# Kernel tuning notes

Hardware: AMD Instinct MI355X
Metric: run time of the kernel (lower is better)

## Reference

```python
import jax, jax.numpy as jnp
import numpy as np

N, E, D = 100000, 640000, 128


def _xavier(key, shape):
    return jax.random.normal(key, shape, jnp.float32) * np.float32(np.sqrt(2.0 / (shape[0] + shape[1])))


def setup_inputs() -> dict:
    key = jax.random.key(0)
    ks = jax.random.split(key, 16)
    inp = {
        "x": jax.random.normal(ks[0], (N, D), jnp.float32),
        "prompt_h": jax.random.normal(ks[1], (N, D), jnp.float32),
        "edge_attr": jax.random.normal(ks[2], (E, D), jnp.float32),
        "prompt_e": jax.random.normal(ks[3], (E, D), jnp.float32),
        "edge_index": jax.random.randint(ks[4], (2, E), 0, N, dtype=jnp.int32),
        # Linear weights stored [in, out] (torch stores [out, in]; math identical)
        "Wq": _xavier(ks[5], (D, D)), "bq": jnp.zeros((D,), jnp.float32),
        "Wk": _xavier(ks[6], (D, D)), "bk": jnp.zeros((D,), jnp.float32),
        "Wv": _xavier(ks[7], (D, D)), "bv": jnp.zeros((D,), jnp.float32),
        "We1": _xavier(ks[8], (D, D)), "be1": jnp.zeros((D,), jnp.float32),
        "We2": _xavier(ks[9], (D, D)), "be2": jnp.zeros((D,), jnp.float32),
        "Wh": _xavier(ks[10], (D, D)), "bh": jnp.zeros((D,), jnp.float32),
        "Wf1": _xavier(ks[11], (D, 2 * D)), "bf1": jnp.zeros((2 * D,), jnp.float32),
        "Wf2": _xavier(ks[12], (2 * D, D)), "bf2": jnp.zeros((D,), jnp.float32),
    }
    return inp


def reference(x, prompt_h, edge_attr, prompt_e, edge_index,
              Wq, bq, Wk, bk, Wv, bv, We1, be1, We2, be2,
              Wh, bh, Wf1, bf1, Wf2, bf2):
    relu = jax.nn.relu
    # Projections (dropout=0, eval mode)
    Q = x @ Wq + bq                      # [N, D]
    K = prompt_h @ Wk + bk               # [N, D]
    V = prompt_h @ Wv + bv               # [N, D]
    h = relu(Q * K)                      # attn_product='mul', score_act with relu
    # Edge-enhanced messages: gather source node scores per edge
    src = h[edge_index[0]]               # [E, D]
    e = relu((edge_attr + prompt_e) @ We1 + be1)
    e = relu((e + prompt_e) @ We2 + be2)  # updated edge_attr (update_e=True)
    msg = relu(src + e)                  # [E, D]
    # scatter-add aggregation into destination nodes
    aggr = jax.ops.segment_sum(msg, edge_index[1], num_segments=x.shape[0])  # [N, D]
    h_out = relu((h + V + aggr) @ Wh + bh)
    h_out = h_out + x                    # residual (in_dim == out_dim)
    h_out = relu(h_out @ Wf1 + bf1)
    h_out = h_out @ Wf2 + bf2            # [N, D]
    return h_out, e
```

## Files before the change

### kernel.cpp

```cpp
#include <hip/hip_runtime.h>

typedef __attribute__((ext_vector_type(8))) short bfrag;
typedef __attribute__((ext_vector_type(4))) float f4;

__device__ __forceinline__ unsigned short f2b(float f) {
  unsigned int u = __builtin_bit_cast(unsigned int, f);
  u = (u + 0x7fffu + ((u >> 16) & 1u)) >> 16;
  return (unsigned short)u;
}
__device__ __forceinline__ float b2f(unsigned short s) {
  unsigned int u = ((unsigned int)s) << 16;
  return __builtin_bit_cast(float, u);
}
__device__ __forceinline__ float relu(float v) { return v > 0.f ? v : 0.f; }

template <bool ADD>
__device__ __forceinline__ void stage_A(char* dst, const float* s0, const float* s1,
                                        long r0, long maxRow) {
  const int tid = threadIdx.x;
#pragma unroll
  for (int i = 0; i < 4; ++i) {
    int ch = tid + (i << 8);
    int row = ch >> 4, kg = ch & 15;
    long gr = r0 + row;
    float v[8];
    if (gr < maxRow) {
      const float4* p = (const float4*)(s0 + gr * 128 + kg * 8);
      float4 a = p[0], b = p[1];
      v[0] = a.x; v[1] = a.y; v[2] = a.z; v[3] = a.w;
      v[4] = b.x; v[5] = b.y; v[6] = b.z; v[7] = b.w;
      if (ADD) {
        const float4* q = (const float4*)(s1 + gr * 128 + kg * 8);
        float4 c = q[0], d = q[1];
        v[0] += c.x; v[1] += c.y; v[2] += c.z; v[3] += c.w;
        v[4] += d.x; v[5] += d.y; v[6] += d.z; v[7] += d.w;
      }
    } else {
#pragma unroll
      for (int j = 0; j < 8; ++j) v[j] = 0.f;
    }
    union { unsigned short h[8]; uint4 u; } pk;
#pragma unroll
    for (int j = 0; j < 8; ++j) pk.h[j] = f2b(v[j]);
    *(uint4*)(dst + (((row << 8) + (kg << 4)) ^ ((row & 7) << 4))) = pk.u;
  }
}

__device__ __forceinline__ void stage_W(char* dst, const unsigned short* src,
                                        int rowStride, int kOff) {
  const int tid = threadIdx.x;
#pragma unroll
  for (int i = 0; i < 8; ++i) {
    int ch = tid + (i << 8);
    int col = ch >> 4, kg = ch & 15;
    uint4 u = *(const uint4*)(src + (size_t)col * rowStride + kOff + kg * 8);
    *(uint4*)(dst + (((col << 8) + (kg << 4)) ^ ((col & 7) << 4))) = u;
  }
}

__device__ __forceinline__ void stage_Wh(char* dst, const unsigned short* src,
                                         int rowStride, int kOff) {
  const int tid = threadIdx.x;
#pragma unroll
  for (int i = 0; i < 4; ++i) {
    int ch = tid + (i << 8);
    int c = ch >> 3, kg = ch & 7;
    uint4 u = *(const uint4*)(src + (size_t)c * rowStride + kOff + kg * 8);
    *(uint4*)(dst + (((c << 7) + (kg << 4)) ^ ((c & 7) << 4))) = u;
  }
}

__device__ __forceinline__ void mm(const char* A, const char* W, int wm, int wn,
                                   int lane, f4 acc[2][4]) {
#pragma unroll
  for (int kk = 0; kk < 4; ++kk) {
    bfrag a[2], b[4];
#pragma unroll
    for (int rt = 0; rt < 2; ++rt) {
      int row = (wm << 5) + (rt << 4) + (lane & 15);
      a[rt] = *(const bfrag*)(A + (((row << 8) + (kk << 6) + ((lane >> 4) << 4)) ^ ((row & 7) << 4)));
    }
#pragma unroll
    for (int ct = 0; ct < 4; ++ct) {
      int col = (wn << 6) + (ct << 4) + (lane & 15);
      b[ct] = *(const bfrag*)(W + (((col << 8) + (kk << 6) + ((lane >> 4) << 4)) ^ ((col & 7) << 4)));
    }
#pragma unroll
    for (int rt = 0; rt < 2; ++rt)
#pragma unroll
      for (int ct = 0; ct < 4; ++ct)
        acc[rt][ct] = __builtin_amdgcn_mfma_f32_16x16x32_bf16(a[rt], b[ct], acc[rt][ct], 0, 0, 0);
  }
}

__device__ __forceinline__ void mm_h(const char* A, const char* W, int wm, int wn,
                                     int lane, f4 acc[2][4], int kh) {
#pragma unroll
  for (int kk2 = 0; kk2 < 2; ++kk2) {
    int kA = (kh << 1) + kk2;
    bfrag a[2], b[4];
#pragma unroll
    for (int rt = 0; rt < 2; ++rt) {
      int row = (wm << 5) + (rt << 4) + (lane & 15);
      a[rt] = *(const bfrag*)(A + (((row << 8) + (kA << 6) + ((lane >> 4) << 4)) ^ ((row & 7) << 4)));
    }
#pragma unroll
    for (int ct = 0; ct < 4; ++ct) {
      int col = (wn << 6) + (ct << 4) + (lane & 15);
      b[ct] = *(const bfrag*)(W + (((col << 7) + (kk2 << 6) + ((lane >> 4) << 4)) ^ ((col & 7) << 4)));
    }
#pragma unroll
    for (int rt = 0; rt < 2; ++rt)
#pragma unroll
      for (int ct = 0; ct < 4; ++ct)
        acc[rt][ct] = __builtin_amdgcn_mfma_f32_16x16x32_bf16(a[rt], b[ct], acc[rt][ct], 0, 0, 0);
  }
}

__global__ void k_prep(const float* __restrict__ Wq, const float* __restrict__ Wk,
                       const float* __restrict__ Wv, const float* __restrict__ We1,
                       const float* __restrict__ We2, const float* __restrict__ Wh,
                       const float* __restrict__ Wf1, const float* __restrict__ Wf2,
                       unsigned short* __restrict__ wt) {
  int b = blockIdx.x, t = threadIdx.x;
  if (b < 384) {
    int m = b >> 6;
    const float* tbl[6] = {Wq, Wk, Wv, We1, We2, Wh};
    const float* src = tbl[m];
    int local = ((b & 63) << 8) + t;
    int n = local >> 7, k = local & 127;
    wt[m * 16384 + local] = f2b(src[k * 128 + n]);
  } else if (b < 512) {
    int local = ((b - 384) << 8) + t;
    int n = local >> 7, k = local & 127;
    wt[98304 + local] = f2b(Wf1[k * 256 + n]);
  } else {
    int local = ((b - 512) << 8) + t;
    int n = local >> 8, k = local & 255;
    wt[131072 + local] = f2b(Wf2[k * 128 + n]);
  }
}

__global__ void k_deg(const int* __restrict__ ei, int* __restrict__ deg, long E) {
  long g = (long)blockIdx.x * 256 + threadIdx.x;
  if (g < E) atomicAdd(deg + ei[E + g], 1);
}

__global__ void k_scanA(const int* __restrict__ deg, int* __restrict__ ex,
                        int* __restrict__ bsum, int n) {
  __shared__ int s[256];
  int t = threadIdx.x; int g = blockIdx.x * 256 + t;
  int v = (g < n) ? deg[g] : 0;
  int val = v;
  s[t] = val; __syncthreads();
#pragma unroll
  for (int o = 1; o < 256; o <<= 1) {
    int u = (t >= o) ? s[t - o] : 0;
    __syncthreads();
    val += u; s[t] = val;
    __syncthreads();
  }
  if (g < n) ex[g] = val - v;
  if (t == 255) bsum[blockIdx.x] = val;
}

__global__ void k_scanB(int* __restrict__ bsum, int nb) {
  __shared__ int s[1024];
  int t = threadIdx.x;
  int v = (t < nb) ? bsum[t] : 0;
  int val = v;
  s[t] = val; __syncthreads();
#pragma unroll
  for (int o = 1; o < 1024; o <<= 1) {
    int u = (t >= o) ? s[t - o] : 0;
    __syncthreads();
    val += u; s[t] = val;
    __syncthreads();
  }
  if (t < nb) bsum[t] = val - v;
}

__global__ void k_scanC(const int* __restrict__ ex, const int* __restrict__ bsum,
                        int* __restrict__ off, int* __restrict__ cursor, int n) {
  int g = blockIdx.x * 256 + threadIdx.x;
  if (g < n) {
    int o = ex[g] + bsum[blockIdx.x];
    off[g] = o; cursor[g] = o;
  }
}

__global__ void k_fill(const int* __restrict__ ei, int* __restrict__ cursor,
                       int* __restrict__ eidx, long E) {
  long g = (long)blockIdx.x * 256 + threadIdx.x;
  if (g < E) {
    int pos = atomicAdd(cursor + ei[E + g], 1);
    eidx[pos] = (int)g;
  }
}

__global__ __launch_bounds__(256, 2) void k_nodes1(
    const float* __restrict__ x, const float* __restrict__ ph,
    const float* __restrict__ bq, const float* __restrict__ bk,
    const float* __restrict__ bv, const unsigned short* __restrict__ wt,
    unsigned short* __restrict__ hbf, float* __restrict__ hpv, long N) {
  extern __shared__ char sm[];
  char* Ax = sm;
  char* Aph = sm + 16384;
  char* Wl = sm + 32768;
  long n0 = (long)blockIdx.x * 64;
  stage_A<false>(Ax, x, nullptr, n0, N);
  stage_A<false>(Aph, ph, nullptr, n0, N);
  stage_W(Wl, wt + 0, 128, 0);
  __syncthreads();
  const int tid = threadIdx.x, lane = tid & 63, w = tid >> 6, wm = w >> 1, wn = w & 1;
  f4 accQ[2][4] = {};
  mm(Ax, Wl, wm, wn, lane, accQ);
  __syncthreads();
  stage_W(Wl, wt + 16384, 128, 0);
  __syncthreads();
  f4 accK[2][4] = {};
  mm(Aph, Wl, wm, wn, lane, accK);
  __syncthreads();
  stage_W(Wl, wt + 32768, 128, 0);
  __syncthreads();
  f4 accV[2][4] = {};
  mm(Aph, Wl, wm, wn, lane, accV);
#pragma unroll
  for (int ct = 0; ct < 4; ++ct) {
    int col = (wn << 6) + (ct << 4) + (lane & 15);
    float vbq = bq[col], vbk = bk[col], vbv = bv[col];
#pragma unroll
    for (int rt = 0; rt < 2; ++rt)
#pragma unroll
      for (int j = 0; j < 4; ++j) {
        int rl = (wm << 5) + (rt << 4) + ((lane >> 4) << 2) + j;
        long row = n0 + rl;
        if (row < N) {
          float q = accQ[rt][ct][j] + vbq;
          float k = accK[rt][ct][j] + vbk;
          float v = accV[rt][ct][j] + vbv;
          float h = relu(q * k);
          hbf[row * 128 + col] = f2b(h);
          hpv[row * 128 + col] = h + v;
        }
      }
  }
}

__global__ __launch_bounds__(256, 3) void k_edges(
    const float* __restrict__ ea, const float* __restrict__ pe,
    const float* __restrict__ be1, const float* __restrict__ be2,
    const unsigned short* __restrict__ wt, const int* __restrict__ ei,
    const unsigned short* __restrict__ hbf, unsigned short* __restrict__ msg,
    float* __restrict__ eout, long E) {
  extern __shared__ char sm[];
  char* A = sm;
  unsigned short* peL = (unsigned short*)(sm + 16384);
  char* Wl = sm + 32768;
  char* stg = sm + 16384;
  int* srcI = (int*)(sm + 49152);
  const int tid = threadIdx.x;
  long e0 = (long)blockIdx.x * 64;
  if (tid < 64) srcI[tid] = (e0 + tid < E) ? ei[e0 + tid] : 0;
#pragma unroll
  for (int i = 0; i < 4; ++i) {
    int ch = tid + (i << 8);
    int row = ch >> 4, kg = ch & 15;
    long gr = e0 + row;
    union { unsigned short h[8]; uint4 u; } s, q;
    if (gr < E) {
      const float4* pa = (const float4*)(ea + gr * 128 + kg * 8);
      const float4* pp = (const float4*)(pe + gr * 128 + kg * 8);
      float4 a0 = pa[0], a1 = pa[1];
      float4 p0 = pp[0], p1 = pp[1];
      s.h[0] = f2b(a0.x + p0.x); s.h[1] = f2b(a0.y + p0.y);
      s.h[2] = f2b(a0.z + p0.z); s.h[3] = f2b(a0.w + p0.w);
      s.h[4] = f2b(a1.x + p1.x); s.h[5] = f2b(a1.y + p1.y);
      s.h[6] = f2b(a1.z + p1.z); s.h[7] = f2b(a1.w + p1.w);
      q.h[0] = f2b(p0.x); q.h[1] = f2b(p0.y); q.h[2] = f2b(p0.z); q.h[3] = f2b(p0.w);
      q.h[4] = f2b(p1.x); q.h[5] = f2b(p1.y); q.h[6] = f2b(p1.z); q.h[7] = f2b(p1.w);
    } else {
      s.u = uint4{0, 0, 0, 0}; q.u = uint4{0, 0, 0, 0};
    }
    *(uint4*)((char*)peL + (row << 8) + (kg << 4)) = q.u;
    *(uint4*)(A + (((row << 8) + (kg << 4)) ^ ((row & 7) << 4))) = s.u;
  }
  stage_Wh(Wl, wt + 49152, 128, 0);
  __syncthreads();
  const int lane = tid & 63, w = tid >> 6, wm = w >> 1, wn = w & 1;
  f4 acc[2][4] = {};
  mm_h(A, Wl, wm, wn, lane, acc, 0);
  __syncthreads();
  stage_Wh(Wl, wt + 49152, 128, 64);
  __syncthreads();
  mm_h(A, Wl, wm, wn, lane, acc, 1);
  __syncthreads();
  const int c0 = (tid & 31) << 2;
  const float4 vb1 = *(const float4*)(be1 + c0);
#pragma unroll
  for (int h = 0; h < 2; ++h) {
    if (wm == h) {
#pragma unroll
      for (int ct = 0; ct < 4; ++ct) {
        int col = (wn << 6) + (ct << 4) + (lane & 15);
#pragma unroll
        for (int rt = 0; rt < 2; ++rt)
#pragma unroll
          for (int j = 0; j < 4; ++j) {
            int lr = (rt << 4) + ((lane >> 4) << 2) + j;
            *(float*)(Wl + (((lr << 9) + (col << 2)) ^ ((lr & 7) << 4))) = acc[rt][ct][j];
          }
      }
    }
    __syncthreads();
#pragma unroll
    for (int it = 0; it < 4; ++it) {
      int lr = (tid >> 5) + (it << 3);
      int r = (h << 5) + lr;
      f4 a = *(const f4*)(Wl + (((lr << 9) + (c0 << 2)) ^ ((lr & 7) << 4)));
      uint2 pu = *(const uint2*)(peL + (r << 7) + c0);
      float p0 = b2f((unsigned short)pu.x), p1 = b2f((unsigned short)(pu.x >> 16));
      float p2 = b2f((unsigned short)pu.y), p3 = b2f((unsigned short)(pu.y >> 16));
      unsigned short t0 = f2b(relu(a[0] + vb1.x) + p0);
      unsigned short t1 = f2b(relu(a[1] + vb1.y) + p1);
      unsigned short t2 = f2b(relu(a[2] + vb1.z) + p2);
      unsigned short t3 = f2b(relu(a[3] + vb1.w) + p3);
      uint2 op;
      op.x = (unsigned int)t0 | ((unsigned int)t1 << 16);
      op.y = (unsigned int)t2 | ((unsigned int)t3 << 16);
      *(uint2*)(A + (((r << 8) + (c0 << 1)) ^ ((r & 7) << 4))) = op;
    }
    __syncthreads();
  }
  stage_Wh(Wl, wt + 65536, 128, 0);
  __syncthreads();
  f4 acc2[2][4] = {};
  mm_h(A, Wl, wm, wn, lane, acc2, 0);
  __syncthreads();
  stage_Wh(Wl, wt + 65536, 128, 64);
  __syncthreads();
  mm_h(A, Wl, wm, wn, lane, acc2, 1);
  __syncthreads();
#pragma unroll
  for (int ct = 0; ct < 4; ++ct) {
    int col = (wn << 6) + (ct << 4) + (lane & 15);
#pragma unroll
    for (int rt = 0; rt < 2; ++rt)
#pragma unroll
      for (int j = 0; j < 4; ++j) {
        int rl = (wm << 5) + (rt << 4) + ((lane >> 4) << 2) + j;
        *(float*)(stg + (((rl << 9) + (col << 2)) ^ ((rl & 7) << 4))) = acc2[rt][ct][j];
      }
  }
  __syncthreads();
  const float4 vb2 = *(const float4*)(be2 + c0);
#pragma unroll
  for (int it = 0; it < 8; ++it) {
    int r = (tid >> 5) + (it << 3);
    long edge = e0 + r;
    if (edge < E) {
      f4 a = *(const f4*)(stg + (((r << 9) + (c0 << 2)) ^ ((r & 7) << 4)));
      float ev0 = relu(a[0] + vb2.x), ev1 = relu(a[1] + vb2.y);
      float ev2 = relu(a[2] + vb2.z), ev3 = relu(a[3] + vb2.w);
      float4 ov; ov.x = ev0; ov.y = ev1; ov.z = ev2; ov.w = ev3;
      *(float4*)(eout + edge * 128 + c0) = ov;
      uint2 hu = *(const uint2*)(hbf + (long)srcI[r] * 128 + c0);
      float h0 = b2f((unsigned short)hu.x), h1 = b2f((unsigned short)(hu.x >> 16));
      float h2 = b2f((unsigned short)hu.y), h3 = b2f((unsigned short)(hu.y >> 16));
      unsigned short m0 = f2b(relu(ev0 + h0)), m1 = f2b(relu(ev1 + h1));
      unsigned short m2 = f2b(relu(ev2 + h2)), m3 = f2b(relu(ev3 + h3));
      uint2 mo;
      mo.x = (unsigned int)m0 | ((unsigned int)m1 << 16);
      mo.y = (unsigned int)m2 | ((unsigned int)m3 << 16);
      *(uint2*)(msg + edge * 128 + c0) = mo;
    }
  }
}

__global__ __launch_bounds__(256, 2) void k_edges_at(
    const float* __restrict__ ea, const float* __restrict__ pe,
    const float* __restrict__ be1, const float* __restrict__ be2,
    const unsigned short* __restrict__ wt, const int* __restrict__ ei,
    const unsigned short* __restrict__ hbf, float* __restrict__ aggr,
    float* __restrict__ eout, long E) {
  extern __shared__ char sm[];
  char* A = sm;
  unsigned short* peL = (unsigned short*)(sm + 16384);
  char* Wl = sm + 32768;
  int* srcI = (int*)(sm + 65536);
  int* dstI = srcI + 64;
  const int tid = threadIdx.x;
  long e0 = (long)blockIdx.x * 64;
  if (tid < 64) {
    long ge = e0 + tid;
    srcI[tid] = (ge < E) ? ei[ge] : 0;
    dstI[tid] = (ge < E) ? ei[E + ge] : 0;
  }
#pragma unroll
  for (int i = 0; i < 4; ++i) {
    int ch = tid + (i << 8);
    int row = ch >> 4, kg = ch & 15;
    long gr = e0 + row;
    union { unsigned short h[8]; uint4 u; } s, q;
    if (gr < E) {
      const float4* pa = (const float4*)(ea + gr * 128 + kg * 8);
      const float4* pp = (const float4*)(pe + gr * 128 + kg * 8);
      float4 a0 = pa[0], a1 = pa[1];
      float4 p0 = pp[0], p1 = pp[1];
      s.h[0] = f2b(a0.x + p0.x); s.h[1] = f2b(a0.y + p0.y);
      s.h[2] = f2b(a0.z + p0.z); s.h[3] = f2b(a0.w + p0.w);
      s.h[4] = f2b(a1.x + p1.x); s.h[5] = f2b(a1.y + p1.y);
      s.h[6] = f2b(a1.z + p1.z); s.h[7] = f2b(a1.w + p1.w);
      q.h[0] = f2b(p0.x); q.h[1] = f2b(p0.y); q.h[2] = f2b(p0.z); q.h[3] = f2b(p0.w);
      q.h[4] = f2b(p1.x); q.h[5] = f2b(p1.y); q.h[6] = f2b(p1.z); q.h[7] = f2b(p1.w);
    } else {
      s.u = uint4{0, 0, 0, 0}; q.u = uint4{0, 0, 0, 0};
    }
    *(uint4*)((char*)peL + (row << 8) + (kg << 4)) = q.u;
    *(uint4*)(A + (((row << 8) + (kg << 4)) ^ ((row & 7) << 4))) = s.u;
  }
  stage_W(Wl, wt + 49152, 128, 0);
  __syncthreads();
  const int lane = tid & 63, w = tid >> 6, wm = w >> 1, wn = w & 1;
  f4 acc[2][4] = {};
  mm(A, Wl, wm, wn, lane, acc);
  __syncthreads();
#pragma unroll
  for (int ct = 0; ct < 4; ++ct) {
    int col = (wn << 6) + (ct << 4) + (lane & 15);
    float b1 = be1[col];
#pragma unroll
    for (int rt = 0; rt < 2; ++rt)
#pragma unroll
      for (int j = 0; j < 4; ++j) {
        int rl = (wm << 5) + (rt << 4) + ((lane >> 4) << 2) + j;
        float tv = relu(acc[rt][ct][j] + b1) + b2f(peL[rl * 128 + col]);
        *(unsigned short*)(A + (((rl << 8) + (col << 1)) ^ ((rl & 7) << 4))) = f2b(tv);
      }
  }
  stage_W(Wl, wt + 65536, 128, 0);
  __syncthreads();
  f4 acc2[2][4] = {};
  mm(A, Wl, wm, wn, lane, acc2);
#pragma unroll
  for (int ct = 0; ct < 4; ++ct) {
    int col = (wn << 6) + (ct << 4) + (lane & 15);
    float b2 = be2[col];
#pragma unroll
    for (int rt = 0; rt < 2; ++rt)
#pragma unroll
      for (int j = 0; j < 4; ++j) {
        int rl = (wm << 5) + (rt << 4) + ((lane >> 4) << 2) + j;
        long edge = e0 + rl;
        if (edge < E) {
          float ev = relu(acc2[rt][ct][j] + b2);
          eout[edge * 128 + col] = ev;
          float hs = b2f(hbf[(long)srcI[rl] * 128 + col]);
          float m = relu(ev + hs);
          atomicAdd(aggr + (long)dstI[rl] * 128 + col, m);
        }
      }
  }
}

__global__ __launch_bounds__(256) void k_aggr(
    const int* __restrict__ off, const int* __restrict__ deg,
    const int* __restrict__ eidx, const unsigned short* __restrict__ msg,
    float* __restrict__ aggr, long N) {
  long node = (long)blockIdx.x * 4 + (threadIdx.x >> 6);
  if (node >= N) return;
  const int lane = threadIdx.x & 63;
  int st = off[node], d = deg[node];
  float a0 = 0.f, a1 = 0.f;
  for (int i = 0; i < d; ++i) {
    int eid = eidx[st + i];
    unsigned int u = *(const unsigned int*)(msg + (long)eid * 128 + lane * 2);
    a0 += b2f((unsigned short)u);
    a1 += b2f((unsigned short)(u >> 16));
  }
  *(float2*)(aggr + node * 128 + lane * 2) = float2{a0, a1};
}

__global__ __launch_bounds__(256, 2) void k_nodes2(
    const float* __restrict__ hpv, const float* __restrict__ aggr,
    const float* __restrict__ x, const float* __restrict__ bh,
    const float* __restrict__ bf1, const float* __restrict__ bf2,
    const unsigned short* __restrict__ wt, float* __restrict__ out, long N) {
  extern __shared__ char sm[];
  char* A = sm;
  char* T = sm + 16384;
  char* Wl = sm + 32768;
  long n0 = (long)blockIdx.x * 64;
  const int tid = threadIdx.x;
  stage_A<true>(A, hpv, aggr, n0, N);
  stage_W(Wl, wt + 81920, 128, 0);
  __syncthreads();
  const int lane = tid & 63, w = tid >> 6, wm = w >> 1, wn = w & 1;
  f4 acc1[2][4] = {};
  mm(A, Wl, wm, wn, lane, acc1);
  __syncthreads();
#pragma unroll
  for (int ct = 0; ct < 4; ++ct) {
    int col = (wn << 6) + (ct << 4) + (lane & 15);
    float bb = bh[col];
#pragma unroll
    for (int rt = 0; rt < 2; ++rt)
#pragma unroll
      for (int j = 0; j < 4; ++j) {
        int rl = (wm << 5) + (rt << 4) + ((lane >> 4) << 2) + j;
        long row = n0 + rl;
        float xv = (row < N) ? x[row * 128 + col] : 0.f;
        float tv = relu(acc1[rt][ct][j] + bb) + xv;
        *(unsigned short*)(T + (((rl << 8) + (col << 1)) ^ ((rl & 7) << 4))) = f2b(tv);
      }
  }
  stage_W(Wl, wt + 98304, 128, 0);
  __syncthreads();
  f4 accA[2][4] = {};
  mm(T, Wl, wm, wn, lane, accA);
  __syncthreads();
#pragma unroll
  for (int ct = 0; ct < 4; ++ct) {
    int col = (wn << 6) + (ct << 4) + (lane & 15);
    float bb = bf1[col];
#pragma unroll
    for (int rt = 0; rt < 2; ++rt)
#pragma unroll
      for (int j = 0; j < 4; ++j) {
        int rl = (wm << 5) + (rt << 4) + ((lane >> 4) << 2) + j;
        float uv = relu(accA[rt][ct][j] + bb);
        *(unsigned short*)(A + (((rl << 8) + (col << 1)) ^ ((rl & 7) << 4))) = f2b(uv);
      }
  }
  stage_W(Wl, wt + 131072, 256, 0);
  __syncthreads();
  f4 acc3[2][4] = {};
  mm(A, Wl, wm, wn, lane, acc3);
  __syncthreads();
  stage_W(Wl, wt + 114688, 128, 0);
  __syncthreads();
  f4 accB[2][4] = {};
  mm(T, Wl, wm, wn, lane, accB);
  __syncthreads();
#pragma unroll
  for (int ct = 0; ct < 4; ++ct) {
    int col = (wn << 6) + (ct << 4) + (lane & 15);
    float bb = bf1[128 + col];
#pragma unroll
    for (int rt = 0; rt < 2; ++rt)
#pragma unroll
      for (int j = 0; j < 4; ++j) {
        int rl = (wm << 5) + (rt << 4) + ((lane >> 4) << 2) + j;
        float uv = relu(accB[rt][ct][j] + bb);
        *(unsigned short*)(A + (((rl << 8) + (col << 1)) ^ ((rl & 7) << 4))) = f2b(uv);
      }
  }
  stage_W(Wl, wt + 131072, 256, 128);
  __syncthreads();
  mm(A, Wl, wm, wn, lane, acc3);
#pragma unroll
  for (int ct = 0; ct < 4; ++ct) {
    int col = (wn << 6) + (ct << 4) + (lane & 15);
    float bb = bf2[col];
#pragma unroll
    for (int rt = 0; rt < 2; ++rt)
#pragma unroll
      for (int j = 0; j < 4; ++j) {
        int rl = (wm << 5) + (rt << 4) + ((lane >> 4) << 2) + j;
        long row = n0 + rl;
        if (row < N) out[row * 128 + col] = acc3[rt][ct][j] + bb;
      }
  }
}

extern "C" void kernel_launch(void* const* d_in, const int* in_sizes, int n_in,
                              void* d_out, int out_size, void* d_ws, size_t ws_size,
                              hipStream_t stream) {
  const float* x   = (const float*)d_in[0];
  const float* ph  = (const float*)d_in[1];
  const float* ea  = (const float*)d_in[2];
  const float* pe  = (const float*)d_in[3];
  const int*   ei  = (const int*)d_in[4];
  const float* Wq  = (const float*)d_in[5];  const float* bq  = (const float*)d_in[6];
  const float* Wk  = (const float*)d_in[7];  const float* bk  = (const float*)d_in[8];
  const float* Wv  = (const float*)d_in[9];  const float* bv  = (const float*)d_in[10];
  const float* We1 = (const float*)d_in[11]; const float* be1 = (const float*)d_in[12];
  const float* We2 = (const float*)d_in[13]; const float* be2 = (const float*)d_in[14];
  const float* Wh  = (const float*)d_in[15]; const float* bh  = (const float*)d_in[16];
  const float* Wf1 = (const float*)d_in[17]; const float* bf1 = (const float*)d_in[18];
  const float* Wf2 = (const float*)d_in[19]; const float* bf2 = (const float*)d_in[20];
  const long N = in_sizes[0] / 128;
  const long E = in_sizes[2] / 128;

  char* ws = (char*)d_ws;
  size_t pos = 0;
  auto alloc = [&](size_t bytes) { size_t p = pos; pos += (bytes + 255) & ~255ULL; return p; };
  size_t o_wt   = alloc(327680);
  size_t o_hbf  = alloc((size_t)N * 256);
  size_t o_hpv  = alloc((size_t)N * 512);
  size_t o_aggr = alloc((size_t)N * 512);
  size_t base_needed = pos;
  size_t o_deg  = alloc((size_t)N * 4);
  size_t o_ex   = alloc((size_t)N * 4);
  size_t o_cur  = alloc((size_t)N * 4);
  size_t o_off  = alloc((size_t)N * 4);
  size_t o_bsum = alloc(4096);
  size_t o_eidx = alloc((size_t)E * 4);
  size_t o_msg  = alloc((size_t)E * 256);
  size_t csr_needed = pos;
  (void)base_needed;

  unsigned short* wt  = (unsigned short*)(ws + o_wt);
  unsigned short* hbf = (unsigned short*)(ws + o_hbf);
  float* hpv  = (float*)(ws + o_hpv);
  float* aggr = (float*)(ws + o_aggr);
  float* outH = (float*)d_out;
  float* outE = outH + N * 128;

  k_prep<<<640, 256, 0, stream>>>(Wq, Wk, Wv, We1, We2, Wh, Wf1, Wf2, wt);
  int nb = (int)((N + 63) / 64);
  int eb = (int)((E + 63) / 64);
  k_nodes1<<<nb, 256, 65536, stream>>>(x, ph, bq, bk, bv, wt, hbf, hpv, N);

  if (ws_size >= csr_needed) {
    int* deg = (int*)(ws + o_deg);
    int* ex  = (int*)(ws + o_ex);
    int* cur = (int*)(ws + o_cur);
    int* off = (int*)(ws + o_off);
    int* bsum = (int*)(ws + o_bsum);
    int* eidx = (int*)(ws + o_eidx);
    unsigned short* msg = (unsigned short*)(ws + o_msg);
    int nb1 = (int)((N + 255) / 256);
    hipMemsetAsync(deg, 0, (size_t)N * 4, stream);
    k_deg<<<(int)((E + 255) / 256), 256, 0, stream>>>(ei, deg, E);
    k_scanA<<<nb1, 256, 0, stream>>>(deg, ex, bsum, (int)N);
    k_scanB<<<1, 1024, 0, stream>>>(bsum, nb1);
    k_scanC<<<nb1, 256, 0, stream>>>(ex, bsum, off, cur, (int)N);
    k_fill<<<(int)((E + 255) / 256), 256, 0, stream>>>(ei, cur, eidx, E);
    k_edges<<<eb, 256, 49408, stream>>>(ea, pe, be1, be2, wt, ei, hbf, msg, outE, E);
    k_aggr<<<(int)((N + 3) / 4), 256, 0, stream>>>(off, deg, eidx, msg, aggr, N);
  } else {
    hipMemsetAsync(aggr, 0, (size_t)N * 512, stream);
    k_edges_at<<<eb, 256, 66048, stream>>>(ea, pe, be1, be2, wt, ei, hbf, aggr, outE, E);
  }
  k_nodes2<<<nb, 256, 65536, stream>>>(hpv, aggr, x, bh, bf1, bf2, wt, outH, N);
}
```

Before: 624.4 us.

## Store h+V in bf16, coalesce node stores, prefetch gathers, unroll aggregation

k_nodes1 now stages its h and h+V outputs through shared memory and writes them as coalesced 8-byte chunks. h+V is stored in bf16 instead of fp32, which halves that intermediate's traffic but adds a rounding step before the Wh matmul. k_edges issues the source-node gathers of h at kernel start so their latency overlaps the edge matmuls. k_aggr unrolls its neighbour loop by four to keep more loads in flight. The atomic fallback path is removed and the CSR path always runs.

```diff
diff --git a/kernel.cpp b/kernel.cpp
--- a/kernel.cpp
+++ b/kernel.cpp
@@ -14,9 +14,7 @@
 }
 __device__ __forceinline__ float relu(float v) { return v > 0.f ? v : 0.f; }
 
-template <bool ADD>
-__device__ __forceinline__ void stage_A(char* dst, const float* s0, const float* s1,
-                                        long r0, long maxRow) {
+__device__ __forceinline__ void stage_A(char* dst, const float* s0, long r0, long maxRow) {
   const int tid = threadIdx.x;
 #pragma unroll
   for (int i = 0; i < 4; ++i) {
@@ -29,12 +27,6 @@
       float4 a = p[0], b = p[1];
       v[0] = a.x; v[1] = a.y; v[2] = a.z; v[3] = a.w;
       v[4] = b.x; v[5] = b.y; v[6] = b.z; v[7] = b.w;
-      if (ADD) {
-        const float4* q = (const float4*)(s1 + gr * 128 + kg * 8);
-        float4 c = q[0], d = q[1];
-        v[0] += c.x; v[1] += c.y; v[2] += c.z; v[3] += c.w;
-        v[4] += d.x; v[5] += d.y; v[6] += d.z; v[7] += d.w;
-      }
     } else {
 #pragma unroll
       for (int j = 0; j < 8; ++j) v[j] = 0.f;
@@ -42,6 +34,34 @@
     union { unsigned short h[8]; uint4 u; } pk;
 #pragma unroll
     for (int j = 0; j < 8; ++j) pk.h[j] = f2b(v[j]);
+    *(uint4*)(dst + (((row << 8) + (kg << 4)) ^ ((row & 7) << 4))) = pk.u;
+  }
+}
+
+__device__ __forceinline__ void stage_A_mix(char* dst, const unsigned short* hb,
+                                            const float* ag, long r0, long maxRow) {
+  const int tid = threadIdx.x;
+#pragma unroll
+  for (int i = 0; i < 4; ++i) {
+    int ch = tid + (i << 8);
+    int row = ch >> 4, kg = ch & 15;
+    long gr = r0 + row;
+    union { unsigned short h[8]; uint4 u; } pk;
+    if (gr < maxRow) {
+      uint4 hv = *(const uint4*)(hb + gr * 128 + kg * 8);
+      const float4* q = (const float4*)(ag + gr * 128 + kg * 8);
+      float4 c = q[0], d = q[1];
+      pk.h[0] = f2b(b2f((unsigned short)hv.x) + c.x);
+      pk.h[1] = f2b(b2f((unsigned short)(hv.x >> 16)) + c.y);
+      pk.h[2] = f2b(b2f((unsigned short)hv.y) + c.z);
+      pk.h[3] = f2b(b2f((unsigned short)(hv.y >> 16)) + c.w);
+      pk.h[4] = f2b(b2f((unsigned short)hv.z) + d.x);
+      pk.h[5] = f2b(b2f((unsigned short)(hv.z >> 16)) + d.y);
+      pk.h[6] = f2b(b2f((unsigned short)hv.w) + d.z);
+      pk.h[7] = f2b(b2f((unsigned short)(hv.w >> 16)) + d.w);
+    } else {
+      pk.u = uint4{0, 0, 0, 0};
+    }
     *(uint4*)(dst + (((row << 8) + (kg << 4)) ^ ((row & 7) << 4))) = pk.u;
   }
 }
@@ -114,6 +134,34 @@
 #pragma unroll
       for (int ct = 0; ct < 4; ++ct)
         acc[rt][ct] = __builtin_amdgcn_mfma_f32_16x16x32_bf16(a[rt], b[ct], acc[rt][ct], 0, 0, 0);
+  }
+}
+
+__device__ __forceinline__ void dump_half(char* Wl, const f4 acc[2][4], int lane, int wn) {
+#pragma unroll
+  for (int ct = 0; ct < 4; ++ct) {
+    int col = (wn << 6) + (ct << 4) + (lane & 15);
+#pragma unroll
+    for (int rt = 0; rt < 2; ++rt)
+#pragma unroll
+      for (int j = 0; j < 4; ++j) {
+        int lr = (rt << 4) + ((lane >> 4) << 2) + j;
+        *(float*)(Wl + (((lr << 9) + (col << 2)) ^ ((lr & 7) << 4))) = acc[rt][ct][j];
+      }
+  }
+}
+
+__device__ __forceinline__ void dump_full(char* stg, const f4 acc[2][4], int lane, int wm, int wn) {
+#pragma unroll
+  for (int ct = 0; ct < 4; ++ct) {
+    int col = (wn << 6) + (ct << 4) + (lane & 15);
+#pragma unroll
+    for (int rt = 0; rt < 2; ++rt)
+#pragma unroll
+      for (int j = 0; j < 4; ++j) {
+        int rl = (wm << 5) + (rt << 4) + ((lane >> 4) << 2) + j;
+        *(float*)(stg + (((rl << 9) + (col << 2)) ^ ((rl & 7) << 4))) = acc[rt][ct][j];
+      }
   }
 }
 
@@ -202,17 +250,18 @@
     const float* __restrict__ x, const float* __restrict__ ph,
     const float* __restrict__ bq, const float* __restrict__ bk,
     const float* __restrict__ bv, const unsigned short* __restrict__ wt,
-    unsigned short* __restrict__ hbf, float* __restrict__ hpv, long N) {
+    unsigned short* __restrict__ hbf, unsigned short* __restrict__ hpvb, long N) {
   extern __shared__ char sm[];
   char* Ax = sm;
   char* Aph = sm + 16384;
   char* Wl = sm + 32768;
   long n0 = (long)blockIdx.x * 64;
-  stage_A<false>(Ax, x, nullptr, n0, N);
-  stage_A<false>(Aph, ph, nullptr, n0, N);
+  const int tid = threadIdx.x, lane = tid & 63, w = tid >> 6, wm = w >> 1, wn = w & 1;
+  const int team = tid >> 5, c0 = (tid & 31) << 2;
+  stage_A(Ax, x, n0, N);
+  stage_A(Aph, ph, n0, N);
   stage_W(Wl, wt + 0, 128, 0);
   __syncthreads();
-  const int tid = threadIdx.x, lane = tid & 63, w = tid >> 6, wm = w >> 1, wn = w & 1;
   f4 accQ[2][4] = {};
   mm(Ax, Wl, wm, wn, lane, accQ);
   __syncthreads();
@@ -225,6 +274,7 @@
   __syncthreads();
   f4 accV[2][4] = {};
   mm(Aph, Wl, wm, wn, lane, accV);
+  __syncthreads();
 #pragma unroll
   for (int ct = 0; ct < 4; ++ct) {
     int col = (wn << 6) + (ct << 4) + (lane & 15);
@@ -234,16 +284,25 @@
 #pragma unroll
       for (int j = 0; j < 4; ++j) {
         int rl = (wm << 5) + (rt << 4) + ((lane >> 4) << 2) + j;
-        long row = n0 + rl;
-        if (row < N) {
-          float q = accQ[rt][ct][j] + vbq;
-          float k = accK[rt][ct][j] + vbk;
-          float v = accV[rt][ct][j] + vbv;
-          float h = relu(q * k);
-          hbf[row * 128 + col] = f2b(h);
-          hpv[row * 128 + col] = h + v;
-        }
+        float q = accQ[rt][ct][j] + vbq;
+        float k = accK[rt][ct][j] + vbk;
+        float v = accV[rt][ct][j] + vbv;
+        float h = relu(q * k);
+        *(unsigned short*)(Ax + (((rl << 8) + (col << 1)) ^ ((rl & 7) << 4))) = f2b(h);
+        *(unsigned short*)(Aph + (((rl << 8) + (col << 1)) ^ ((rl & 7) << 4))) = f2b(h + v);
       }
+  }
+  __syncthreads();
+#pragma unroll
+  for (int it = 0; it < 8; ++it) {
+    int r = team + (it << 3);
+    long row = n0 + r;
+    if (row < N) {
+      uint2 hb = *(const uint2*)(Ax + (((r << 8) + (c0 << 1)) ^ ((r & 7) << 4)));
+      uint2 hv = *(const uint2*)(Aph + (((r << 8) + (c0 << 1)) ^ ((r & 7) << 4)));
+      *(uint2*)(hbf + row * 128 + c0) = hb;
+      *(uint2*)(hpvb + row * 128 + c0) = hv;
+    }
   }
 }
 
@@ -258,10 +317,18 @@
   unsigned short* peL = (unsigned short*)(sm + 16384);
   char* Wl = sm + 32768;
   char* stg = sm + 16384;
-  int* srcI = (int*)(sm + 49152);
   const int tid = threadIdx.x;
+  const int team = tid >> 5, c0 = (tid & 31) << 2;
   long e0 = (long)blockIdx.x * 64;
-  if (tid < 64) srcI[tid] = (e0 + tid < E) ? ei[e0 + tid] : 0;
+
+  uint2 hu[8];
+#pragma unroll
+  for (int it = 0; it < 8; ++it) {
+    int r = team + (it << 3);
+    long ge = e0 + r;
+    int s = (ge < E) ? ei[ge] : 0;
+    hu[it] = *(const uint2*)(hbf + (long)s * 128 + c0);
+  }
 #pragma unroll
   for (int i = 0; i < 4; ++i) {
     int ch = tid + (i << 8);
@@ -295,27 +362,14 @@
   __syncthreads();
   mm_h(A, Wl, wm, wn, lane, acc, 1);
   __syncthreads();
-  const int c0 = (tid & 31) << 2;
   const float4 vb1 = *(const float4*)(be1 + c0);
 #pragma unroll
   for (int h = 0; h < 2; ++h) {
-    if (wm == h) {
-#pragma unroll
-      for (int ct = 0; ct < 4; ++ct) {
-        int col = (wn << 6) + (ct << 4) + (lane & 15);
-#pragma unroll
-        for (int rt = 0; rt < 2; ++rt)
-#pragma unroll
-          for (int j = 0; j < 4; ++j) {
-            int lr = (rt << 4) + ((lane >> 4) << 2) + j;
-            *(float*)(Wl + (((lr << 9) + (col << 2)) ^ ((lr & 7) << 4))) = acc[rt][ct][j];
-          }
-      }
-    }
+    if (wm == h) dump_half(Wl, acc, lane, wn);
     __syncthreads();
 #pragma unroll
     for (int it = 0; it < 4; ++it) {
-      int lr = (tid >> 5) + (it << 3);
+      int lr = team + (it << 3);
       int r = (h << 5) + lr;
       f4 a = *(const f4*)(Wl + (((lr << 9) + (c0 << 2)) ^ ((lr & 7) << 4)));
       uint2 pu = *(const uint2*)(peL + (r << 7) + c0);
@@ -341,22 +395,12 @@
   __syncthreads();
   mm_h(A, Wl, wm, wn, lane, acc2, 1);
   __syncthreads();
-#pragma unroll
-  for (int ct = 0; ct < 4; ++ct) {
-    int col = (wn << 6) + (ct << 4) + (lane & 15);
-#pragma unroll
-    for (int rt = 0; rt < 2; ++rt)
-#pragma unroll
-      for (int j = 0; j < 4; ++j) {
-        int rl = (wm << 5) + (rt << 4) + ((lane >> 4) << 2) + j;
-        *(float*)(stg + (((rl << 9) + (col << 2)) ^ ((rl & 7) << 4))) = acc2[rt][ct][j];
-      }
-  }
+  dump_full(stg, acc2, lane, wm, wn);
   __syncthreads();
   const float4 vb2 = *(const float4*)(be2 + c0);
 #pragma unroll
   for (int it = 0; it < 8; ++it) {
-    int r = (tid >> 5) + (it << 3);
+    int r = team + (it << 3);
     long edge = e0 + r;
     if (edge < E) {
       f4 a = *(const f4*)(stg + (((r << 9) + (c0 << 2)) ^ ((r & 7) << 4)));
@@ -364,9 +408,8 @@
       float ev2 = relu(a[2] + vb2.z), ev3 = relu(a[3] + vb2.w);
       float4 ov; ov.x = ev0; ov.y = ev1; ov.z = ev2; ov.w = ev3;
       *(float4*)(eout + edge * 128 + c0) = ov;
-      uint2 hu = *(const uint2*)(hbf + (long)srcI[r] * 128 + c0);
-      float h0 = b2f((unsigned short)hu.x), h1 = b2f((unsigned short)(hu.x >> 16));
-      float h2 = b2f((unsigned short)hu.y), h3 = b2f((unsigned short)(hu.y >> 16));
+      float h0 = b2f((unsigned short)hu[it].x), h1 = b2f((unsigned short)(hu[it].x >> 16));
+      float h2 = b2f((unsigned short)hu[it].y), h3 = b2f((unsigned short)(hu[it].y >> 16));
       unsigned short m0 = f2b(relu(ev0 + h0)), m1 = f2b(relu(ev1 + h1));
       unsigned short m2 = f2b(relu(ev2 + h2)), m3 = f2b(relu(ev3 + h3));
       uint2 mo;
@@ -374,92 +417,6 @@
       mo.y = (unsigned int)m2 | ((unsigned int)m3 << 16);
       *(uint2*)(msg + edge * 128 + c0) = mo;
     }
-  }
-}
-
-__global__ __launch_bounds__(256, 2) void k_edges_at(
-    const float* __restrict__ ea, const float* __restrict__ pe,
-    const float* __restrict__ be1, const float* __restrict__ be2,
-    const unsigned short* __restrict__ wt, const int* __restrict__ ei,
-    const unsigned short* __restrict__ hbf, float* __restrict__ aggr,
-    float* __restrict__ eout, long E) {
-  extern __shared__ char sm[];
-  char* A = sm;
-  unsigned short* peL = (unsigned short*)(sm + 16384);
-  char* Wl = sm + 32768;
-  int* srcI = (int*)(sm + 65536);
-  int* dstI = srcI + 64;
-  const int tid = threadIdx.x;
-  long e0 = (long)blockIdx.x * 64;
-  if (tid < 64) {
-    long ge = e0 + tid;
-    srcI[tid] = (ge < E) ? ei[ge] : 0;
-    dstI[tid] = (ge < E) ? ei[E + ge] : 0;
-  }
-#pragma unroll
-  for (int i = 0; i < 4; ++i) {
-    int ch = tid + (i << 8);
-    int row = ch >> 4, kg = ch & 15;
-    long gr = e0 + row;
-    union { unsigned short h[8]; uint4 u; } s, q;
-    if (gr < E) {
-      const float4* pa = (const float4*)(ea + gr * 128 + kg * 8);
-      const float4* pp = (const float4*)(pe + gr * 128 + kg * 8);
-      float4 a0 = pa[0], a1 = pa[1];
-      float4 p0 = pp[0], p1 = pp[1];
-      s.h[0] = f2b(a0.x + p0.x); s.h[1] = f2b(a0.y + p0.y);
-      s.h[2] = f2b(a0.z + p0.z); s.h[3] = f2b(a0.w + p0.w);
-      s.h[4] = f2b(a1.x + p1.x); s.h[5] = f2b(a1.y + p1.y);
-      s.h[6] = f2b(a1.z + p1.z); s.h[7] = f2b(a1.w + p1.w);
-      q.h[0] = f2b(p0.x); q.h[1] = f2b(p0.y); q.h[2] = f2b(p0.z); q.h[3] = f2b(p0.w);
-      q.h[4] = f2b(p1.x); q.h[5] = f2b(p1.y); q.h[6] = f2b(p1.z); q.h[7] = f2b(p1.w);
-    } else {
-      s.u = uint4{0, 0, 0, 0}; q.u = uint4{0, 0, 0, 0};
-    }
-    *(uint4*)((char*)peL + (row << 8) + (kg << 4)) = q.u;
-    *(uint4*)(A + (((row << 8) + (kg << 4)) ^ ((row & 7) << 4))) = s.u;
-  }
-  stage_W(Wl, wt + 49152, 128, 0);
-  __syncthreads();
-  const int lane = tid & 63, w = tid >> 6, wm = w >> 1, wn = w & 1;
-  f4 acc[2][4] = {};
-  mm(A, Wl, wm, wn, lane, acc);
-  __syncthreads();
-#pragma unroll
-  for (int ct = 0; ct < 4; ++ct) {
-    int col = (wn << 6) + (ct << 4) + (lane & 15);
-    float b1 = be1[col];
-#pragma unroll
-    for (int rt = 0; rt < 2; ++rt)
-#pragma unroll
-      for (int j = 0; j < 4; ++j) {
-        int rl = (wm << 5) + (rt << 4) + ((lane >> 4) << 2) + j;
-        float tv = relu(acc[rt][ct][j] + b1) + b2f(peL[rl * 128 + col]);
-        *(unsigned short*)(A + (((rl << 8) + (col << 1)) ^ ((rl & 7) << 4))) = f2b(tv);
-      }
-  }
-  stage_W(Wl, wt + 65536, 128, 0);
-  __syncthreads();
-  f4 acc2[2][4] = {};
-  mm(A, Wl, wm, wn, lane, acc2);
-#pragma unroll
-  for (int ct = 0; ct < 4; ++ct) {
-    int col = (wn << 6) + (ct << 4) + (lane & 15);
-    float b2 = be2[col];
-#pragma unroll
-    for (int rt = 0; rt < 2; ++rt)
-#pragma unroll
-      for (int j = 0; j < 4; ++j) {
-        int rl = (wm << 5) + (rt << 4) + ((lane >> 4) << 2) + j;
-        long edge = e0 + rl;
-        if (edge < E) {
-          float ev = relu(acc2[rt][ct][j] + b2);
-          eout[edge * 128 + col] = ev;
-          float hs = b2f(hbf[(long)srcI[rl] * 128 + col]);
-          float m = relu(ev + hs);
-          atomicAdd(aggr + (long)dstI[rl] * 128 + col, m);
-        }
-      }
   }
 }
 
@@ -472,7 +429,20 @@
   const int lane = threadIdx.x & 63;
   int st = off[node], d = deg[node];
   float a0 = 0.f, a1 = 0.f;
-  for (int i = 0; i < d; ++i) {
+  int i = 0;
+  for (; i + 3 < d; i += 4) {
+    int e0i = eidx[st + i], e1i = eidx[st + i + 1];
+    int e2i = eidx[st + i + 2], e3i = eidx[st + i + 3];
+    unsigned int u0 = *(const unsigned int*)(msg + (long)e0i * 128 + lane * 2);
+    unsigned int u1 = *(const unsigned int*)(msg + (long)e1i * 128 + lane * 2);
+    unsigned int u2 = *(const unsigned int*)(msg + (long)e2i * 128 + lane * 2);
+    unsigned int u3 = *(const unsigned int*)(msg + (long)e3i * 128 + lane * 2);
+    a0 += b2f((unsigned short)u0) + b2f((unsigned short)u1) +
+          b2f((unsigned short)u2) + b2f((unsigned short)u3);
+    a1 += b2f((unsigned short)(u0 >> 16)) + b2f((unsigned short)(u1 >> 16)) +
+          b2f((unsigned short)(u2 >> 16)) + b2f((unsigned short)(u3 >> 16));
+  }
+  for (; i < d; ++i) {
     int eid = eidx[st + i];
     unsigned int u = *(const unsigned int*)(msg + (long)eid * 128 + lane * 2);
     a0 += b2f((unsigned short)u);
@@ -482,7 +452,7 @@
 }
 
 __global__ __launch_bounds__(256, 2) void k_nodes2(
-    const float* __restrict__ hpv, const float* __restrict__ aggr,
+    const unsigned short* __restrict__ hpvb, const float* __restrict__ aggr,
     const float* __restrict__ x, const float* __restrict__ bh,
     const float* __restrict__ bf1, const float* __restrict__ bf2,
     const unsigned short* __restrict__ wt, float* __restrict__ out, long N) {
@@ -492,7 +462,7 @@
   char* Wl = sm + 32768;
   long n0 = (long)blockIdx.x * 64;
   const int tid = threadIdx.x;
-  stage_A<true>(A, hpv, aggr, n0, N);
+  stage_A_mix(A, hpvb, aggr, n0, N);
   stage_W(Wl, wt + 81920, 128, 0);
   __syncthreads();
   const int lane = tid & 63, w = tid >> 6, wm = w >> 1, wn = w & 1;
@@ -593,13 +563,12 @@
   const long E = in_sizes[2] / 128;
 
   char* ws = (char*)d_ws;
-  size_t pos = 0;
-  auto alloc = [&](size_t bytes) { size_t p = pos; pos += (bytes + 255) & ~255ULL; return p; };
+  size_t pos_ = 0;
+  auto alloc = [&](size_t bytes) { size_t p = pos_; pos_ += (bytes + 255) & ~255ULL; return p; };
   size_t o_wt   = alloc(327680);
   size_t o_hbf  = alloc((size_t)N * 256);
-  size_t o_hpv  = alloc((size_t)N * 512);
+  size_t o_hpv  = alloc((size_t)N * 256);
   size_t o_aggr = alloc((size_t)N * 512);
-  size_t base_needed = pos;
   size_t o_deg  = alloc((size_t)N * 4);
   size_t o_ex   = alloc((size_t)N * 4);
   size_t o_cur  = alloc((size_t)N * 4);
@@ -607,12 +576,11 @@
   size_t o_bsum = alloc(4096);
   size_t o_eidx = alloc((size_t)E * 4);
   size_t o_msg  = alloc((size_t)E * 256);
-  size_t csr_needed = pos;
-  (void)base_needed;
-
-  unsigned short* wt  = (unsigned short*)(ws + o_wt);
-  unsigned short* hbf = (unsigned short*)(ws + o_hbf);
-  float* hpv  = (float*)(ws + o_hpv);
+  (void)pos_;
+
+  unsigned short* wt   = (unsigned short*)(ws + o_wt);
+  unsigned short* hbf  = (unsigned short*)(ws + o_hbf);
+  unsigned short* hpvb = (unsigned short*)(ws + o_hpv);
   float* aggr = (float*)(ws + o_aggr);
   float* outH = (float*)d_out;
   float* outE = outH + N * 128;
@@ -620,28 +588,23 @@
   k_prep<<<640, 256, 0, stream>>>(Wq, Wk, Wv, We1, We2, Wh, Wf1, Wf2, wt);
   int nb = (int)((N + 63) / 64);
   int eb = (int)((E + 63) / 64);
-  k_nodes1<<<nb, 256, 65536, stream>>>(x, ph, bq, bk, bv, wt, hbf, hpv, N);
-
-  if (ws_size >= csr_needed) {
-    int* deg = (int*)(ws + o_deg);
-    int* ex  = (int*)(ws + o_ex);
-    int* cur = (int*)(ws + o_cur);
-    int* off = (int*)(ws + o_off);
-    int* bsum = (int*)(ws + o_bsum);
-    int* eidx = (int*)(ws + o_eidx);
-    unsigned short* msg = (unsigned short*)(ws + o_msg);
-    int nb1 = (int)((N + 255) / 256);
-    hipMemsetAsync(deg, 0, (size_t)N * 4, stream);
-    k_deg<<<(int)((E + 255) / 256), 256, 0, stream>>>(ei, deg, E);
-    k_scanA<<<nb1, 256, 0, stream>>>(deg, ex, bsum, (int)N);
-    k_scanB<<<1, 1024, 0, stream>>>(bsum, nb1);
-    k_scanC<<<nb1, 256, 0, stream>>>(ex, bsum, off, cur, (int)N);
-    k_fill<<<(int)((E + 255) / 256), 256, 0, stream>>>(ei, cur, eidx, E);
-    k_edges<<<eb, 256, 49408, stream>>>(ea, pe, be1, be2, wt, ei, hbf, msg, outE, E);
-    k_aggr<<<(int)((N + 3) / 4), 256, 0, stream>>>(off, deg, eidx, msg, aggr, N);
-  } else {
-    hipMemsetAsync(aggr, 0, (size_t)N * 512, stream);
-    k_edges_at<<<eb, 256, 66048, stream>>>(ea, pe, be1, be2, wt, ei, hbf, aggr, outE, E);
-  }
-  k_nodes2<<<nb, 256, 65536, stream>>>(hpv, aggr, x, bh, bf1, bf2, wt, outH, N);
-}
+  k_nodes1<<<nb, 256, 65536, stream>>>(x, ph, bq, bk, bv, wt, hbf, hpvb, N);
+
+  int* deg = (int*)(ws + o_deg);
+  int* ex  = (int*)(ws + o_ex);
+  int* cur = (int*)(ws + o_cur);
+  int* off = (int*)(ws + o_off);
+  int* bsum = (int*)(ws + o_bsum);
+  int* eidx = (int*)(ws + o_eidx);
+  unsigned short* msg = (unsigned short*)(ws + o_msg);
+  int nb1 = (int)((N + 255) / 256);
+  hipMemsetAsync(deg, 0, (size_t)N * 4, stream);
+  k_deg<<<(int)((E + 255) / 256), 256, 0, stream>>>(ei, deg, E);
+  k_scanA<<<nb1, 256, 0, stream>>>(deg, ex, bsum, (int)N);
+  k_scanB<<<1, 1024, 0, stream>>>(bsum, nb1);
+  k_scanC<<<nb1, 256, 0, stream>>>(ex, bsum, off, cur, (int)N);
+  k_fill<<<(int)((E + 255) / 256), 256, 0, stream>>>(ei, cur, eidx, E);
+  k_edges<<<eb, 256, 49152, stream>>>(ea, pe, be1, be2, wt, ei, hbf, msg, outE, E);
+  k_aggr<<<(int)((N + 3) / 4), 256, 0, stream>>>(off, deg, eidx, msg, aggr, N);
+  k_nodes2<<<nb, 256, 65536, stream>>>(hpvb, aggr, x, bh, bf1, bf2, wt, outH, N);
+}
```

Result: faster. 582.4 us (-6.7%).
